# Performance work log

Hardware: AMD Instinct MI355X
Metric: run time of the kernel (lower is better)

Reference implementation:

```python
import jax, jax.numpy as jnp
import numpy as np

S = 20  # amino-acid alphabet size
B, L, H, K, NUM_RATES = 1024, 512, 2, 2, 100000


def make_R(kernel):
    # symmetric, positive, zero-diagonal exchangeability matrices (H,k,20,20)
    R = 0.5 * (kernel + jnp.swapaxes(kernel, -1, -2))
    R = jax.nn.softplus(R)
    return R * (1.0 - jnp.eye(S, dtype=R.dtype))


def make_p(kernel):
    # equilibrium distributions (H,k,20)
    return jax.nn.softmax(kernel, axis=-1)


def make_rate_matrix(R, p, eps=1e-16):
    # Q_ij = R_ij * p_j ; diagonal set so rows sum to 0; normalized to 1
    # expected mutation per unit time.
    Q = R * p[..., None, :]
    row = jnp.sum(Q, axis=-1)                      # (...,20)
    Q = Q - row[..., :, None] * jnp.eye(S, dtype=Q.dtype)
    mue = jnp.sum(p * row, axis=-1)[..., None, None]
    return Q / jnp.maximum(mue, eps)


def expm_gtr(Q, p, tau):
    # GTR expm via symmetric eigendecomposition:
    # Sm = diag(sqrt(p)) Q diag(1/sqrt(p)) is symmetric; e^{tQ} =
    # diag(1/sqrt(p)) U e^{t*lam} U^T diag(sqrt(p)).
    sqrt_p = jnp.sqrt(p)                           # (H,k,20)
    inv_sqrt_p = 1.0 / sqrt_p
    Sm = sqrt_p[..., :, None] * Q * inv_sqrt_p[..., None, :]
    Sm = 0.5 * (Sm + jnp.swapaxes(Sm, -1, -2))     # enforce symmetry
    lam, U = jnp.linalg.eigh(Sm)                   # (H,k,20), (H,k,20,20)
    E = jnp.exp(tau[:, :, None, None] * lam[None])  # (B,H,k,20)
    M = jnp.einsum('hkis,bhks,hkjs->bhkij', U, E, U)
    P = inv_sqrt_p[None, :, :, :, None] * M * sqrt_p[None, :, :, None, :]
    return P                                       # (B,H,k,20,20)


def setup_inputs() -> dict:
    key = jax.random.key(0)
    k1, k2, k3, k4, k5 = jax.random.split(key, 5)
    labels = jax.random.randint(k1, (B, L, H), 0, S)
    inputs = jax.nn.one_hot(labels, S, dtype=jnp.float32)        # (B,L,H,20)
    rate_indices = jax.random.randint(k2, (B, H), 0, NUM_RATES)  # (B,H)
    tau_kernel = -3.0 + 0.1 * jax.random.normal(k3, (H, NUM_RATES), jnp.float32)
    exchangeability_kernel = 0.1 * jax.random.normal(k4, (H, K, S, S), jnp.float32)
    equilibrium_kernel = 0.1 * jax.random.normal(k5, (H, K, S), jnp.float32)
    return {
        'inputs': inputs,
        'rate_indices': rate_indices,
        'tau_kernel': tau_kernel,
        'exchangeability_kernel': exchangeability_kernel,
        'equilibrium_kernel': equilibrium_kernel,
    }


def reference(inputs, rate_indices, tau_kernel, exchangeability_kernel, equilibrium_kernel):
    # tau per (sequence, model): tau_kernel[h, rate_indices[b,h]], softplus branch lengths
    h_idx = jnp.arange(H)[None, :]
    tau = jax.nn.softplus(tau_kernel[h_idx, rate_indices])       # (B,H)
    R = make_R(exchangeability_kernel)                           # (H,k,20,20)
    p = make_p(equilibrium_kernel)                               # (H,k,20)
    Q = make_rate_matrix(R, p)                                   # (H,k,20,20)
    P = expm_gtr(Q, p, tau)                                      # (B,H,k,20,20)
    # ancestral probabilities (transposed=False): 'bLmz,bmkzs->bLmks'
    ancprobs = jnp.einsum('blhz,bhkzs->blhks', inputs, P)
    return ancprobs                                              # (B,L,H,k,20)
```

## Files before the change

### kernel.cpp

```cpp
#include <hip/hip_runtime.h>
#include <math.h>

#define S20 20
#define BB 1024
#define LL 512
#define HH 2
#define KK 2
#define NRATES 100000
#define NTERM 10

__device__ __forceinline__ float softplusf(float x) {
    if (x > 20.f) return x;
    return log1pf(expf(x));
}

__global__ __launch_bounds__(256) void build_qpow(
        const float* __restrict__ exch,
        const float* __restrict__ eq,
        float* __restrict__ qpow) {
    __shared__ float p[S20];
    __shared__ float row[S20];
    __shared__ float mue_s;
    __shared__ float Qm[400];
    __shared__ float bufA[400];
    __shared__ float bufB[400];

    const int hk = blockIdx.x;
    const int tid = threadIdx.x;

    if (tid == 0) {
        const float* e = eq + hk * S20;
        float m = -1e30f;
        for (int i = 0; i < S20; i++) m = fmaxf(m, e[i]);
        float s = 0.f;
        for (int i = 0; i < S20; i++) { float v = expf(e[i] - m); p[i] = v; s += v; }
        float inv = 1.f / s;
        for (int i = 0; i < S20; i++) p[i] *= inv;
    }
    __syncthreads();

    const float* ek = exch + hk * 400;
    for (int e = tid; e < 400; e += 256) {
        int i = e / 20, j = e % 20;
        float r = 0.f;
        if (i != j) r = softplusf(0.5f * (ek[i * 20 + j] + ek[j * 20 + i]));
        Qm[e] = r * p[j];
    }
    __syncthreads();

    if (tid < S20) {
        float s = 0.f;
        for (int j = 0; j < S20; j++) s += Qm[tid * 20 + j];
        row[tid] = s;
    }
    __syncthreads();
    if (tid == 0) {
        float m = 0.f;
        for (int i = 0; i < S20; i++) m += p[i] * row[i];
        mue_s = fmaxf(m, 1e-16f);
    }
    __syncthreads();

    const float inv_mue = 1.f / mue_s;
    for (int e = tid; e < 400; e += 256) {
        int i = e / 20, j = e % 20;
        float q = Qm[e];
        if (i == j) q -= row[i];
        Qm[e] = q * inv_mue;
    }
    __syncthreads();

    float* outb = qpow + (size_t)hk * (NTERM + 1) * 400;
    for (int e = tid; e < 400; e += 256) {
        int i = e / 20, j = e % 20;
        outb[e]        = (i == j) ? 1.f : 0.f;
        outb[400 + e]  = Qm[e];
        bufA[e]        = Qm[e];
    }
    __syncthreads();

    float* cur = bufA;
    float* nxt = bufB;
    for (int n = 2; n <= NTERM; n++) {
        float invn = 1.f / (float)n;
        for (int e = tid; e < 400; e += 256) {
            int i = e / 20, j = e % 20;
            float acc = 0.f;
#pragma unroll
            for (int s = 0; s < S20; s++)
                acc += cur[i * 20 + s] * Qm[s * 20 + j];
            acc *= invn;
            nxt[e] = acc;
            outb[(size_t)n * 400 + e] = acc;
        }
        __syncthreads();
        float* t = cur; cur = nxt; nxt = t;
    }
}

__global__ __launch_bounds__(256) void anc_probs(
        const float* __restrict__ inputs,
        const int*   __restrict__ rate_indices,
        const float* __restrict__ tau_kernel,
        const float* __restrict__ qpow,
        float* __restrict__ out) {
    __shared__ __align__(16) float P[4 * 400];
    __shared__ int zb[LL * HH];
    __shared__ float tauv[HH];

    const int b = blockIdx.x;
    const int tid = threadIdx.x;

    if (tid < HH) {
        int ridx = rate_indices[b * HH + tid];
        tauv[tid] = softplusf(tau_kernel[tid * NRATES + ridx]);
    }
    __syncthreads();

    for (int e = tid; e < 1600; e += 256) {
        int hk = e / 400;
        int h  = hk >> 1;
        int ij = e % 400;
        float tau = tauv[h];
        const float* cb = qpow + (size_t)hk * (NTERM + 1) * 400 + ij;
        float acc = cb[NTERM * 400];
#pragma unroll
        for (int n = NTERM - 1; n >= 0; n--)
            acc = acc * tau + cb[n * 400];
        P[e] = acc;
    }

    const float* inB = inputs + (size_t)b * LL * HH * S20;
    for (int r = tid; r < LL * HH; r += 256) {
        const float4* rp = (const float4*)(inB + r * S20);
        int z = 0;
#pragma unroll
        for (int q = 0; q < 5; q++) {
            float4 v = rp[q];
            int base = q * 4;
            if (v.x > 0.5f) z = base;
            if (v.y > 0.5f) z = base + 1;
            if (v.z > 0.5f) z = base + 2;
            if (v.w > 0.5f) z = base + 3;
        }
        zb[r] = z;
    }
    __syncthreads();

    float4* outB = (float4*)(out + (size_t)b * LL * HH * KK * S20);
    for (int f = tid; f < 10240; f += 256) {
        int l  = f / 20;
        int r  = f % 20;
        int h  = r / 10;
        int k  = (r % 10) / 5;
        int s4 = r % 5;
        int z  = zb[l * HH + h];
        float4 v = *(const float4*)(&P[(h * 2 + k) * 400 + z * 20 + s4 * 4]);
        outB[f] = v;
    }
}

extern "C" void kernel_launch(void* const* d_in, const int* in_sizes, int n_in,
                              void* d_out, int out_size, void* d_ws, size_t ws_size,
                              hipStream_t stream) {
    const float* inputs       = (const float*)d_in[0];
    const int*   rate_indices = (const int*)  d_in[1];
    const float* tau_kernel   = (const float*)d_in[2];
    const float* exch         = (const float*)d_in[3];
    const float* eq           = (const float*)d_in[4];
    float* out  = (float*)d_out;
    float* qpow = (float*)d_ws;

    build_qpow<<<dim3(HH * KK), dim3(256), 0, stream>>>(exch, eq, qpow);
    anc_probs<<<dim3(BB), dim3(256), 0, stream>>>(inputs, rate_indices,
                                                  tau_kernel, qpow, out);
}
```

Before: 250.2 us.

## Split each sequence across two blocks, coalesce input scan, use nontemporal stores

Each batch row is now handled by two blocks, each covering half of the L positions, which doubles the grid and halves the per-block work. The one-hot input scan now reads fully coalesced float4 lanes, one vector per thread, instead of each thread reading a whole 20-float row. Output writes use nontemporal stores to avoid polluting cache with the large streaming output. In exchange, each block still recomputes the full 4x400 P matrix, so that work is duplicated twice as often.

```diff
diff --git a/kernel.cpp b/kernel.cpp
--- a/kernel.cpp
+++ b/kernel.cpp
@@ -8,6 +8,8 @@
 #define KK 2
 #define NRATES 100000
 #define NTERM 10
+
+typedef float v4f __attribute__((ext_vector_type(4)));
 
 __device__ __forceinline__ float softplusf(float x) {
     if (x > 20.f) return x;
@@ -105,11 +107,13 @@
         const float* __restrict__ qpow,
         float* __restrict__ out) {
     __shared__ __align__(16) float P[4 * 400];
-    __shared__ int zb[LL * HH];
+    __shared__ int zb[512];
     __shared__ float tauv[HH];
 
-    const int b = blockIdx.x;
-    const int tid = threadIdx.x;
+    const int blk  = blockIdx.x;
+    const int b    = blk >> 1;
+    const int half = blk & 1;
+    const int tid  = threadIdx.x;
 
     if (tid < HH) {
         int ridx = rate_indices[b * HH + tid];
@@ -130,33 +134,30 @@
         P[e] = acc;
     }
 
-    const float* inB = inputs + (size_t)b * LL * HH * S20;
-    for (int r = tid; r < LL * HH; r += 256) {
-        const float4* rp = (const float4*)(inB + r * S20);
-        int z = 0;
-#pragma unroll
-        for (int q = 0; q < 5; q++) {
-            float4 v = rp[q];
-            int base = q * 4;
-            if (v.x > 0.5f) z = base;
-            if (v.y > 0.5f) z = base + 1;
-            if (v.z > 0.5f) z = base + 2;
-            if (v.w > 0.5f) z = base + 3;
-        }
-        zb[r] = z;
+    const v4f* inB = (const v4f*)(inputs
+                        + (size_t)b * (LL * HH * S20) + (size_t)half * 10240);
+    for (int f = tid; f < 2560; f += 256) {
+        v4f v = inB[f];
+        int row   = f / 5;
+        int zbase = (f % 5) * 4;
+        if (v.x > 0.5f) zb[row] = zbase;
+        if (v.y > 0.5f) zb[row] = zbase + 1;
+        if (v.z > 0.5f) zb[row] = zbase + 2;
+        if (v.w > 0.5f) zb[row] = zbase + 3;
     }
     __syncthreads();
 
-    float4* outB = (float4*)(out + (size_t)b * LL * HH * KK * S20);
-    for (int f = tid; f < 10240; f += 256) {
+    v4f* outB = (v4f*)(out + (size_t)b * (LL * HH * KK * S20)
+                           + (size_t)half * 20480);
+    for (int f = tid; f < 5120; f += 256) {
         int l  = f / 20;
         int r  = f % 20;
         int h  = r / 10;
         int k  = (r % 10) / 5;
         int s4 = r % 5;
         int z  = zb[l * HH + h];
-        float4 v = *(const float4*)(&P[(h * 2 + k) * 400 + z * 20 + s4 * 4]);
-        outB[f] = v;
+        v4f v = *(const v4f*)(&P[(h * 2 + k) * 400 + z * 20 + s4 * 4]);
+        __builtin_nontemporal_store(v, outB + f);
     }
 }
 
@@ -172,6 +173,6 @@
     float* qpow = (float*)d_ws;
 
     build_qpow<<<dim3(HH * KK), dim3(256), 0, stream>>>(exch, eq, qpow);
-    anc_probs<<<dim3(BB), dim3(256), 0, stream>>>(inputs, rate_indices,
-                                                  tau_kernel, qpow, out);
+    anc_probs<<<dim3(BB * 2), dim3(256), 0, stream>>>(inputs, rate_indices,
+                                                      tau_kernel, qpow, out);
 }
```

Measured after the change: 252.4 us. No clear change (+0.9%).
